# Kernel optimization log

Measured on AMD Instinct MI355X. Metric: run time of the kernel, lower is better.

## Reference

```python
import jax, jax.numpy as jnp
import numpy as np

N = 100000      # nodes
IN = 64         # in_channels
HID = 64        # hidden_channels
H2 = HID // 2   # per-sign channels
E = 1600000     # edges per sign


def _mean_aggr(x_src, edge_index, num_nodes):
    """Mean of x_src[src] scattered onto dst (PyG mean aggregation)."""
    src, dst = edge_index[0], edge_index[1]
    s = jax.ops.segment_sum(x_src[src], dst, num_segments=num_nodes)
    cnt = jax.ops.segment_sum(jnp.ones((src.shape[0],), x_src.dtype), dst,
                              num_segments=num_nodes)
    return s / jnp.maximum(cnt, 1.0)[:, None]


def setup_inputs() -> dict:
    key = jax.random.key(0)
    ks = jax.random.split(key, 12)
    x = jax.random.normal(ks[0], (N, IN), jnp.float32)
    pos_edge_index = jax.random.randint(ks[1], (2, E), 0, N)
    neg_edge_index = jax.random.randint(ks[2], (2, E), 0, N)

    def w(k, fan_in, fan_out):
        b = 1.0 / np.sqrt(fan_in)
        return jax.random.uniform(k, (fan_in, fan_out), jnp.float32, -b, b)

    return dict(
        x=x, pos_edge_index=pos_edge_index, neg_edge_index=neg_edge_index,
        # conv1 (first_aggr=True): lin_l (no bias applied via l), lin_r (bias)
        w1_pl=w(ks[3], IN, H2), w1_pr=w(ks[4], IN, H2), b1_p=jnp.zeros((H2,), jnp.float32),
        w1_nl=w(ks[5], IN, H2), w1_nr=w(ks[6], IN, H2), b1_n=jnp.zeros((H2,), jnp.float32),
        # conv2 (first_aggr=False): lin_l over cat of two aggregations (2*H2), lin_r over H2
        w2_pl=w(ks[7], 2 * H2, H2), w2_pr=w(ks[8], H2, H2), b2_p=jnp.zeros((H2,), jnp.float32),
        w2_nl=w(ks[9], 2 * H2, H2), w2_nr=w(ks[10], H2, H2), b2_n=jnp.zeros((H2,), jnp.float32),
    )


def reference(x, pos_edge_index, neg_edge_index,
              w1_pl, w1_pr, b1_p, w1_nl, w1_nr, b1_n,
              w2_pl, w2_pr, b2_p, w2_nl, w2_nr, b2_n):
    n = x.shape[0]
    # --- conv1, first_aggr=True ---
    agg_p = _mean_aggr(x, pos_edge_index, n)          # [N, IN]
    agg_n = _mean_aggr(x, neg_edge_index, n)
    out_pos = agg_p @ w1_pl + x @ w1_pr + b1_p         # [N, H2]
    out_neg = agg_n @ w1_nl + x @ w1_nr + b1_n
    z = jax.nn.relu(jnp.concatenate([out_pos, out_neg], axis=-1))  # [N, HID]

    # --- conv2, first_aggr=False ---
    h2 = z.shape[-1] // 2
    zp, zn = z[:, :h2], z[:, h2:]
    p1 = _mean_aggr(zp, pos_edge_index, n)
    p2 = _mean_aggr(zn, neg_edge_index, n)
    out_pos = jnp.concatenate([p1, p2], axis=-1) @ w2_pl + zp @ w2_pr + b2_p
    n1 = _mean_aggr(zn, pos_edge_index, n)
    n2 = _mean_aggr(zp, neg_edge_index, n)
    out_neg = jnp.concatenate([n1, n2], axis=-1) @ w2_nl + zn @ w2_nr + b2_n
    z = jax.nn.relu(jnp.concatenate([out_pos, out_neg], axis=-1))  # [N, HID]
    return z
```

## Files before the change

kernel.cpp:

```cpp
#include <hip/hip_runtime.h>
#include <hip/hip_fp16.h>

using uint = unsigned int;

static constexpr int NN  = 100000;
static constexpr int NE  = 1600000;
static constexpr int DIM = 64;
static constexpr int HH  = 32;
static constexpr int NBLK = (NN + 255) / 256;
static constexpr int HB   = 256;
static constexpr int CHUNK = NE / HB;
static constexpr int BSH  = 8;
static constexpr int BSZ  = 256;
static constexpr int NBKT = (NN + BSZ - 1) / BSZ;

__device__ __forceinline__ float2 up16(uint v) {
  __half2 h = *reinterpret_cast<__half2*>(&v);
  return __half22float2(h);
}
__device__ __forceinline__ uint pk16(float a, float b) {
  __half2 h = __floats2half2_rn(a, b);
  return *reinterpret_cast<uint*>(&h);
}


__global__ void c_hist(const int* __restrict__ pe, const int* __restrict__ ne,
                       int* __restrict__ part_hist) {
  const int set = blockIdx.y;
  const int* dstA = (set ? ne : pe) + NE;
  __shared__ int h[512];
  h[threadIdx.x] = 0; h[threadIdx.x + 256] = 0;
  __syncthreads();
  int lo = blockIdx.x * CHUNK;
  int hi = lo + CHUNK;
  for (int i = lo + threadIdx.x; i < hi; i += 256)
    atomicAdd(&h[dstA[i] >> BSH], 1);
  __syncthreads();
  int* o = part_hist + (size_t)(set * HB + blockIdx.x) * 512;
  o[threadIdx.x] = h[threadIdx.x];
  o[threadIdx.x + 256] = h[threadIdx.x + 256];
}

__global__ void c_colscan(int* __restrict__ part_hist, int* __restrict__ tot) {
  const int set = blockIdx.y;
  const int k   = blockIdx.x;
  const int t   = threadIdx.x;
  int v = part_hist[(size_t)(set * HB + t) * 512 + k];
  __shared__ int sm[256];
  sm[t] = v;
  __syncthreads();
  for (int off = 1; off < 256; off <<= 1) {
    int add = (t >= off) ? sm[t - off] : 0;
    __syncthreads();
    sm[t] += add;
    __syncthreads();
  }
  part_hist[(size_t)(set * HB + t) * 512 + k] = (t == 0) ? 0 : sm[t - 1];
  if (t == 255) tot[set * 512 + k] = sm[255];
}

__global__ void c_basescan(const int* __restrict__ tot, int* __restrict__ base) {
  const int t   = threadIdx.x;
  const int seg = t >> 9;
  const int idx = t & 511;
  int v = tot[seg * 512 + idx];
  __shared__ int sm[1024];
  sm[t] = v;
  __syncthreads();
  for (int off = 1; off < 512; off <<= 1) {
    int add = (idx >= off) ? sm[t - off] : 0;
    __syncthreads();
    sm[t] += add;
    __syncthreads();
  }
  base[seg * 513 + idx] = (idx == 0) ? 0 : sm[t - 1];
  if (idx == 511) base[seg * 513 + 512] = sm[t];
}

__global__ void c_scatpre(const int* __restrict__ pe, const int* __restrict__ ne,
                          const int* __restrict__ part_hist, const int* __restrict__ base,
                          uint* __restrict__ partP, uint* __restrict__ partN,
                          const float* __restrict__ x,
                          const float* __restrict__ w1_pl, const float* __restrict__ w1_pr,
                          const float* __restrict__ b1_p,
                          const float* __restrict__ w1_nl, const float* __restrict__ w1_nr,
                          const float* __restrict__ b1_n,
                          uint* __restrict__ y1p, uint* __restrict__ y1n,
                          float* __restrict__ r1) {
  __shared__ uint smem[4096];
  const int bx = blockIdx.x;
  const int t  = threadIdx.x;

  if (bx < 512) {
    const int set = bx >> 8;
    const int b   = bx & 255;
    const int* srcA = set ? ne : pe;
    const int* dstA = srcA + NE;
    uint* part = set ? partN : partP;
    int* off = (int*)smem;
    const int* ph = part_hist + (size_t)(set * HB + b) * 512;
    off[t]       = base[set * 513 + t]       + ph[t];
    off[t + 256] = base[set * 513 + t + 256] + ph[t + 256];
    __syncthreads();
    int lo = b * CHUNK;
    int hi = lo + CHUNK;
    for (int i = lo + t; i < hi; i += 256) {
      int src = srcA[i];
      int dst = dstA[i];
      int pos = atomicAdd(&off[dst >> BSH], 1);
      part[pos] = ((uint)src << BSH) | (uint)(dst & (BSZ - 1));
    }
    return;
  }

  const int pb   = bx - 512;
  const int h    = (pb >= NBLK) ? 1 : 0;
  const int nblk = pb - (h ? NBLK : 0);
  const float* wl   = h ? w1_nl : w1_pl;
  const float* wr   = h ? w1_nr : w1_pr;
  const float* bias = h ? b1_n  : b1_p;

  float* s_wl = (float*)smem;
  float* s_wr = (float*)smem + 2048;
  for (int i = t; i < DIM * HH; i += 256) {
    s_wl[i] = wl[i];
    s_wr[i] = wr[i];
  }
  __syncthreads();

  int node = nblk * 256 + t;
  if (node >= NN) return;

  float ay[HH], ar[HH];
#pragma unroll
  for (int j = 0; j < HH; ++j) { ay[j] = 0.f; ar[j] = bias[j]; }

  const float4* xrow = (const float4*)(x + (size_t)node * DIM);
#pragma unroll 4
  for (int k4 = 0; k4 < DIM / 4; ++k4) {
    float4 xv = xrow[k4];
#pragma unroll
    for (int u = 0; u < 4; ++u) {
      int k = k4 * 4 + u;
      float xk = (&xv.x)[u];
#pragma unroll
      for (int j = 0; j < HH; ++j) {
        ay[j] += xk * s_wl[k * HH + j];
        ar[j] += xk * s_wr[k * HH + j];
      }
    }
  }

  uint*  yo = (h ? y1n : y1p) + (size_t)node * 16;
  float* ro = r1 + (size_t)node * 64 + h * 32;
#pragma unroll
  for (int j = 0; j < 16; ++j) yo[j] = pk16(ay[2 * j], ay[2 * j + 1]);
#pragma unroll
  for (int j = 0; j < HH; ++j) ro[j] = ar[j];
}

__global__ void c_bucket(const uint* __restrict__ partP, const uint* __restrict__ partN,
                         const int* __restrict__ base,
                         int* __restrict__ row_p, int* __restrict__ row_n,
                         int* __restrict__ col_p, int* __restrict__ col_n) {
  const int bx = blockIdx.x;
  const int t  = threadIdx.x;
  const int set = (bx >= NBKT) ? 1 : 0;
  const int k   = bx - (set ? NBKT : 0);
  const uint* part = set ? partN : partP;
  int* row = set ? row_n : row_p;
  int* col = set ? col_n : col_p;
  const int lo = k * BSZ;
  const int hi = min(lo + BSZ, NN);
  const int s = base[set * 513 + k];
  const int e = base[set * 513 + k + 1];

  __shared__ int cnt[BSZ], rowl[BSZ], cnt2[BSZ];
  cnt[t] = 0; cnt2[t] = 0;
  __syncthreads();
  for (int i = s + t; i < e; i += 256)
    atomicAdd(&cnt[part[i] & (BSZ - 1)], 1);
  __syncthreads();
  rowl[t] = cnt[t];
  __syncthreads();
  for (int off = 1; off < BSZ; off <<= 1) {
    int a0 = (t >= off) ? rowl[t - off] : 0;
    __syncthreads();
    rowl[t] += a0;
    __syncthreads();
  }
  if (lo + t < hi) row[lo + t] = s + (t ? rowl[t - 1] : 0);
  if (k == NBKT - 1 && t == 0) row[NN] = NE;
  for (int i = s + t; i < e; i += 256) {
    uint p = part[i];
    int l = p & (BSZ - 1);
    int pos = s + (l ? rowl[l - 1] : 0) + atomicAdd(&cnt2[l], 1);
    col[pos] = (int)(p >> BSH);
  }
}

__global__ void k_aggr1(const uint* __restrict__ y1p, const uint* __restrict__ y1n,
                        const int* __restrict__ rp, const int* __restrict__ cp,
                        const int* __restrict__ rn, const int* __restrict__ cn,
                        const float* r1,
                        float* z) {
  int gid  = blockIdx.x * 256 + threadIdx.x;
  int node = gid >> 6;
  if (node >= NN) return;
  int lane = threadIdx.x & 63;
  int g = lane >> 2;
  int f = lane & 3;

  int s = rp[node], e = rp[node + 1];
  float a[8];
#pragma unroll
  for (int j = 0; j < 8; ++j) a[j] = 0.f;
  for (int i = s + g; i < e; i += 16) {
    int c = cp[i];
    uint4 v = *(const uint4*)&y1p[(size_t)c * 16 + 4 * f];
    float2 p0 = up16(v.x), p1 = up16(v.y), p2 = up16(v.z), p3 = up16(v.w);
    a[0] += p0.x; a[1] += p0.y; a[2] += p1.x; a[3] += p1.y;
    a[4] += p2.x; a[5] += p2.y; a[6] += p3.x; a[7] += p3.y;
  }
#pragma unroll
  for (int w = 4; w <= 32; w <<= 1) {
#pragma unroll
    for (int j = 0; j < 8; ++j) a[j] += __shfl_xor(a[j], w);
  }
  float invp = 1.f / (float)max(e - s, 1);

  s = rn[node]; e = rn[node + 1];
  float b[8];
#pragma unroll
  for (int j = 0; j < 8; ++j) b[j] = 0.f;
  for (int i = s + g; i < e; i += 16) {
    int c = cn[i];
    uint4 v = *(const uint4*)&y1n[(size_t)c * 16 + 4 * f];
    float2 p0 = up16(v.x), p1 = up16(v.y), p2 = up16(v.z), p3 = up16(v.w);
    b[0] += p0.x; b[1] += p0.y; b[2] += p1.x; b[3] += p1.y;
    b[4] += p2.x; b[5] += p2.y; b[6] += p3.x; b[7] += p3.y;
  }
#pragma unroll
  for (int w = 4; w <= 32; w <<= 1) {
#pragma unroll
    for (int j = 0; j < 8; ++j) b[j] += __shfl_xor(b[j], w);
  }
  float invn = 1.f / (float)max(e - s, 1);

  size_t base = (size_t)node * 64;
  if (g == 0) {
    const float4 r0 = *(const float4*)(r1 + base + 8 * f);
    const float4 r1v = *(const float4*)(r1 + base + 8 * f + 4);
    float4 o0, o1;
    o0.x = fmaxf(a[0] * invp + r0.x, 0.f);
    o0.y = fmaxf(a[1] * invp + r0.y, 0.f);
    o0.z = fmaxf(a[2] * invp + r0.z, 0.f);
    o0.w = fmaxf(a[3] * invp + r0.w, 0.f);
    o1.x = fmaxf(a[4] * invp + r1v.x, 0.f);
    o1.y = fmaxf(a[5] * invp + r1v.y, 0.f);
    o1.z = fmaxf(a[6] * invp + r1v.z, 0.f);
    o1.w = fmaxf(a[7] * invp + r1v.w, 0.f);
    *(float4*)(z + base + 8 * f) = o0;
    *(float4*)(z + base + 8 * f + 4) = o1;
  } else if (g == 1) {
    const float4 r0 = *(const float4*)(r1 + base + 32 + 8 * f);
    const float4 r1v = *(const float4*)(r1 + base + 32 + 8 * f + 4);
    float4 o0, o1;
    o0.x = fmaxf(b[0] * invn + r0.x, 0.f);
    o0.y = fmaxf(b[1] * invn + r0.y, 0.f);
    o0.z = fmaxf(b[2] * invn + r0.z, 0.f);
    o0.w = fmaxf(b[3] * invn + r0.w, 0.f);
    o1.x = fmaxf(b[4] * invn + r1v.x, 0.f);
    o1.y = fmaxf(b[5] * invn + r1v.y, 0.f);
    o1.z = fmaxf(b[6] * invn + r1v.z, 0.f);
    o1.w = fmaxf(b[7] * invn + r1v.w, 0.f);
    *(float4*)(z + base + 32 + 8 * f) = o0;
    *(float4*)(z + base + 32 + 8 * f + 4) = o1;
  }
}

__global__ void k_mid(const float* __restrict__ z,
                      const float* __restrict__ w2_pl, const float* __restrict__ w2_pr,
                      const float* __restrict__ b2_p,
                      const float* __restrict__ w2_nl, const float* __restrict__ w2_nr,
                      const float* __restrict__ b2_n,
                      uint* __restrict__ u_pos, uint* __restrict__ u_neg,
                      float* __restrict__ r2) {
  const int t = blockIdx.y;
  const float* mat;
  const float* bias = nullptr;
  int srcHalf;
  switch (t) {
    case 0: mat = w2_pl;            srcHalf = 0; break;
    case 1: mat = w2_nl;            srcHalf = 1; break;
    case 2: mat = w2_pl + 32 * 32;  srcHalf = 1; break;
    case 3: mat = w2_nl + 32 * 32;  srcHalf = 0; break;
    case 4: mat = w2_pr; bias = b2_p; srcHalf = 0; break;
    default: mat = w2_nr; bias = b2_n; srcHalf = 1; break;
  }

  __shared__ float s_m[HH][HH];
  for (int i = threadIdx.x; i < HH * HH; i += 256) s_m[i >> 5][i & 31] = mat[i];
  __syncthreads();

  int node = blockIdx.x * 256 + threadIdx.x;
  if (node >= NN) return;

  float acc[HH];
#pragma unroll
  for (int j = 0; j < HH; ++j) acc[j] = bias ? bias[j] : 0.f;

  const float4* zrow = (const float4*)(z + (size_t)node * 64 + srcHalf * 32);
#pragma unroll 4
  for (int k4 = 0; k4 < HH / 4; ++k4) {
    float4 v = zrow[k4];
#pragma unroll
    for (int u = 0; u < 4; ++u) {
      int k = k4 * 4 + u;
      float vv = (&v.x)[u];
#pragma unroll
      for (int j = 0; j < HH; ++j) acc[j] += vv * s_m[k][j];
    }
  }

  if (t < 4) {
    uint* o = (t < 2 ? u_pos : u_neg) + (size_t)node * 32 + (t & 1) * 16;
#pragma unroll
    for (int j = 0; j < 16; ++j) o[j] = pk16(acc[2 * j], acc[2 * j + 1]);
  } else {
    float* o = r2 + (size_t)node * 64 + (t - 4) * 32;
#pragma unroll
    for (int j = 0; j < HH; ++j) o[j] = acc[j];
  }
}

__global__ void k_aggr2(const uint* __restrict__ u_pos, const uint* __restrict__ u_neg,
                        const int* __restrict__ rp, const int* __restrict__ cp,
                        const int* __restrict__ rn, const int* __restrict__ cn,
                        const float* __restrict__ r2,
                        float* __restrict__ out) {
  int gid  = blockIdx.x * 256 + threadIdx.x;
  int node = gid >> 6;
  if (node >= NN) return;
  int lane = threadIdx.x & 63;
  int g = lane >> 3;
  int f = lane & 7;

  int s = rp[node], e = rp[node + 1];
  float a[8];
#pragma unroll
  for (int j = 0; j < 8; ++j) a[j] = 0.f;
  for (int i = s + g; i < e; i += 8) {
    int c = cp[i];
    uint4 v = *(const uint4*)&u_pos[(size_t)c * 32 + 4 * f];
    float2 p0 = up16(v.x), p1 = up16(v.y), p2 = up16(v.z), p3 = up16(v.w);
    a[0] += p0.x; a[1] += p0.y; a[2] += p1.x; a[3] += p1.y;
    a[4] += p2.x; a[5] += p2.y; a[6] += p3.x; a[7] += p3.y;
  }
#pragma unroll
  for (int w = 8; w <= 32; w <<= 1) {
#pragma unroll
    for (int j = 0; j < 8; ++j) a[j] += __shfl_xor(a[j], w);
  }
  float invp = 1.f / (float)max(e - s, 1);

  s = rn[node]; e = rn[node + 1];
  float b[8];
#pragma unroll
  for (int j = 0; j < 8; ++j) b[j] = 0.f;
  for (int i = s + g; i < e; i += 8) {
    int c = cn[i];
    uint4 v = *(const uint4*)&u_neg[(size_t)c * 32 + 4 * f];
    float2 p0 = up16(v.x), p1 = up16(v.y), p2 = up16(v.z), p3 = up16(v.w);
    b[0] += p0.x; b[1] += p0.y; b[2] += p1.x; b[3] += p1.y;
    b[4] += p2.x; b[5] += p2.y; b[6] += p3.x; b[7] += p3.y;
  }
#pragma unroll
  for (int w = 8; w <= 32; w <<= 1) {
#pragma unroll
    for (int j = 0; j < 8; ++j) b[j] += __shfl_xor(b[j], w);
  }
  float invn = 1.f / (float)max(e - s, 1);

  if (g == 0) {
    size_t base = (size_t)node * 64 + 8 * f;
    const float4 r0 = *(const float4*)(r2 + base);
    const float4 r1v = *(const float4*)(r2 + base + 4);
    float4 o0, o1;
    o0.x = fmaxf(a[0] * invp + b[0] * invn + r0.x, 0.f);
    o0.y = fmaxf(a[1] * invp + b[1] * invn + r0.y, 0.f);
    o0.z = fmaxf(a[2] * invp + b[2] * invn + r0.z, 0.f);
    o0.w = fmaxf(a[3] * invp + b[3] * invn + r0.w, 0.f);
    o1.x = fmaxf(a[4] * invp + b[4] * invn + r1v.x, 0.f);
    o1.y = fmaxf(a[5] * invp + b[5] * invn + r1v.y, 0.f);
    o1.z = fmaxf(a[6] * invp + b[6] * invn + r1v.z, 0.f);
    o1.w = fmaxf(a[7] * invp + b[7] * invn + r1v.w, 0.f);
    *(float4*)(out + base) = o0;
    *(float4*)(out + base + 4) = o1;
  }
}


extern "C" void kernel_launch(void* const* d_in, const int* in_sizes, int n_in,
                              void* d_out, int out_size, void* d_ws, size_t ws_size,
                              hipStream_t stream) {
  const float* x     = (const float*)d_in[0];
  const int*   pe    = (const int*)d_in[1];
  const int*   ne    = (const int*)d_in[2];
  const float* w1_pl = (const float*)d_in[3];
  const float* w1_pr = (const float*)d_in[4];
  const float* b1_p  = (const float*)d_in[5];
  const float* w1_nl = (const float*)d_in[6];
  const float* w1_nr = (const float*)d_in[7];
  const float* b1_n  = (const float*)d_in[8];
  const float* w2_pl = (const float*)d_in[9];
  const float* w2_pr = (const float*)d_in[10];
  const float* b2_p  = (const float*)d_in[11];
  const float* w2_nl = (const float*)d_in[12];
  const float* w2_nr = (const float*)d_in[13];
  const float* b2_n  = (const float*)d_in[14];

  char* ws = (char*)d_ws;
  size_t off = 0;
  auto alloc = [&](size_t bytes) -> char* {
    char* p = ws + off;
    off = (off + bytes + 255) & ~(size_t)255;
    return p;
  };

  int* row_p = (int*)alloc((size_t)(NN + 1) * 4);
  int* row_n = (int*)alloc((size_t)(NN + 1) * 4);
  int* col_p = (int*)alloc((size_t)NE * 4);
  int* col_n = (int*)alloc((size_t)NE * 4);
  int* part_hist = (int*)alloc((size_t)2 * HB * 512 * 4);
  int* tot   = (int*)alloc((size_t)2 * 512 * 4);
  int* base  = (int*)alloc((size_t)2 * 513 * 4);

  char* regA  = alloc((size_t)NN * 64 * 4);
  uint* partP = (uint*)regA;
  uint* partN = (uint*)(regA + (size_t)NE * 4);
  uint* u_pos = (uint*)regA;
  uint* u_neg = (uint*)(regA + (size_t)NN * 32 * 4);

  char*  regB = alloc((size_t)NN * 64 * 4);
  uint*  y1p  = (uint*)regB;
  uint*  y1n  = (uint*)(regB + (size_t)NN * 16 * 4);
  float* r2   = (float*)regB;

  float* r1 = (float*)d_out;
  float* z  = (float*)d_out;

  const int nb = NBLK;
  const int ab = (NN * 64 + 255) / 256;

  dim3 hg(HB, 2);
  c_hist<<<hg, 256, 0, stream>>>(pe, ne, part_hist);
  dim3 cg(512, 2);
  c_colscan<<<cg, 256, 0, stream>>>(part_hist, tot);
  c_basescan<<<1, 1024, 0, stream>>>(tot, base);
  c_scatpre<<<512 + 2 * NBLK, 256, 0, stream>>>(
      pe, ne, part_hist, base, partP, partN,
      x, w1_pl, w1_pr, b1_p, w1_nl, w1_nr, b1_n, y1p, y1n, r1);
  c_bucket<<<2 * NBKT, 256, 0, stream>>>(partP, partN, base,
                                         row_p, row_n, col_p, col_n);

  k_aggr1<<<ab, 256, 0, stream>>>(y1p, y1n, row_p, col_p, row_n, col_n, r1, z);

  dim3 g2(nb, 6);
  k_mid<<<g2, 256, 0, stream>>>(z, w2_pl, w2_pr, b2_p, w2_nl, w2_nr, b2_n,
                                u_pos, u_neg, r2);

  k_aggr2<<<ab, 256, 0, stream>>>(u_pos, u_neg, row_p, col_p, row_n, col_n, r2,
                                  (float*)d_out);
}
```

Measured before the change: 304.0 us.

## Use more histogram/scatter blocks and split layer-1 precompute into its own kernel

Raises the number of edge-partition blocks from 256 to 1024 per sign, so the histogram and scatter passes spread across more CUs with smaller chunks, and widens the column scan to 1024 threads. The layer-1 dense transform is pulled out of the combined scatter kernel into a separate kernel launched first, so the scatter no longer shares a grid with divergent matmul blocks. part_hist moves into the regA workspace region after the partition buffers. The larger histogram costs more scan work and memory, and there is one extra launch.

After: 330.3 us. 1.09x slower.

```diff
diff --git a/kernel.cpp b/kernel.cpp
--- a/kernel.cpp
+++ b/kernel.cpp
@@ -8,8 +8,8 @@
 static constexpr int DIM = 64;
 static constexpr int HH  = 32;
 static constexpr int NBLK = (NN + 255) / 256;
-static constexpr int HB   = 256;
-static constexpr int CHUNK = NE / HB;
+static constexpr int HB   = 1024;
+static constexpr int CHUNK = (NE + HB - 1) / HB;
 static constexpr int BSH  = 8;
 static constexpr int BSZ  = 256;
 static constexpr int NBKT = (NN + BSZ - 1) / BSZ;
@@ -32,7 +32,7 @@
   h[threadIdx.x] = 0; h[threadIdx.x + 256] = 0;
   __syncthreads();
   int lo = blockIdx.x * CHUNK;
-  int hi = lo + CHUNK;
+  int hi = min(lo + CHUNK, NE);
   for (int i = lo + threadIdx.x; i < hi; i += 256)
     atomicAdd(&h[dstA[i] >> BSH], 1);
   __syncthreads();
@@ -46,17 +46,17 @@
   const int k   = blockIdx.x;
   const int t   = threadIdx.x;
   int v = part_hist[(size_t)(set * HB + t) * 512 + k];
-  __shared__ int sm[256];
+  __shared__ int sm[HB];
   sm[t] = v;
   __syncthreads();
-  for (int off = 1; off < 256; off <<= 1) {
+  for (int off = 1; off < HB; off <<= 1) {
     int add = (t >= off) ? sm[t - off] : 0;
     __syncthreads();
     sm[t] += add;
     __syncthreads();
   }
   part_hist[(size_t)(set * HB + t) * 512 + k] = (t == 0) ? 0 : sm[t - 1];
-  if (t == 255) tot[set * 512 + k] = sm[255];
+  if (t == HB - 1) tot[set * 512 + k] = sm[HB - 1];
 }
 
 __global__ void c_basescan(const int* __restrict__ tot, int* __restrict__ base) {
@@ -77,86 +77,27 @@
   if (idx == 511) base[seg * 513 + 512] = sm[t];
 }
 
-__global__ void c_scatpre(const int* __restrict__ pe, const int* __restrict__ ne,
+__global__ void c_scatter(const int* __restrict__ pe, const int* __restrict__ ne,
                           const int* __restrict__ part_hist, const int* __restrict__ base,
-                          uint* __restrict__ partP, uint* __restrict__ partN,
-                          const float* __restrict__ x,
-                          const float* __restrict__ w1_pl, const float* __restrict__ w1_pr,
-                          const float* __restrict__ b1_p,
-                          const float* __restrict__ w1_nl, const float* __restrict__ w1_nr,
-                          const float* __restrict__ b1_n,
-                          uint* __restrict__ y1p, uint* __restrict__ y1n,
-                          float* __restrict__ r1) {
-  __shared__ uint smem[4096];
-  const int bx = blockIdx.x;
-  const int t  = threadIdx.x;
-
-  if (bx < 512) {
-    const int set = bx >> 8;
-    const int b   = bx & 255;
-    const int* srcA = set ? ne : pe;
-    const int* dstA = srcA + NE;
-    uint* part = set ? partN : partP;
-    int* off = (int*)smem;
-    const int* ph = part_hist + (size_t)(set * HB + b) * 512;
-    off[t]       = base[set * 513 + t]       + ph[t];
-    off[t + 256] = base[set * 513 + t + 256] + ph[t + 256];
-    __syncthreads();
-    int lo = b * CHUNK;
-    int hi = lo + CHUNK;
-    for (int i = lo + t; i < hi; i += 256) {
-      int src = srcA[i];
-      int dst = dstA[i];
-      int pos = atomicAdd(&off[dst >> BSH], 1);
-      part[pos] = ((uint)src << BSH) | (uint)(dst & (BSZ - 1));
-    }
-    return;
-  }
-
-  const int pb   = bx - 512;
-  const int h    = (pb >= NBLK) ? 1 : 0;
-  const int nblk = pb - (h ? NBLK : 0);
-  const float* wl   = h ? w1_nl : w1_pl;
-  const float* wr   = h ? w1_nr : w1_pr;
-  const float* bias = h ? b1_n  : b1_p;
-
-  float* s_wl = (float*)smem;
-  float* s_wr = (float*)smem + 2048;
-  for (int i = t; i < DIM * HH; i += 256) {
-    s_wl[i] = wl[i];
-    s_wr[i] = wr[i];
-  }
-  __syncthreads();
-
-  int node = nblk * 256 + t;
-  if (node >= NN) return;
-
-  float ay[HH], ar[HH];
-#pragma unroll
-  for (int j = 0; j < HH; ++j) { ay[j] = 0.f; ar[j] = bias[j]; }
-
-  const float4* xrow = (const float4*)(x + (size_t)node * DIM);
-#pragma unroll 4
-  for (int k4 = 0; k4 < DIM / 4; ++k4) {
-    float4 xv = xrow[k4];
-#pragma unroll
-    for (int u = 0; u < 4; ++u) {
-      int k = k4 * 4 + u;
-      float xk = (&xv.x)[u];
-#pragma unroll
-      for (int j = 0; j < HH; ++j) {
-        ay[j] += xk * s_wl[k * HH + j];
-        ar[j] += xk * s_wr[k * HH + j];
-      }
-    }
-  }
-
-  uint*  yo = (h ? y1n : y1p) + (size_t)node * 16;
-  float* ro = r1 + (size_t)node * 64 + h * 32;
-#pragma unroll
-  for (int j = 0; j < 16; ++j) yo[j] = pk16(ay[2 * j], ay[2 * j + 1]);
-#pragma unroll
-  for (int j = 0; j < HH; ++j) ro[j] = ar[j];
+                          uint* __restrict__ partP, uint* __restrict__ partN) {
+  const int set = blockIdx.y;
+  const int b   = blockIdx.x;
+  const int* srcA = set ? ne : pe;
+  const int* dstA = srcA + NE;
+  uint* part = set ? partN : partP;
+  __shared__ int off[512];
+  const int* ph = part_hist + (size_t)(set * HB + b) * 512;
+  off[threadIdx.x]       = base[set * 513 + threadIdx.x]       + ph[threadIdx.x];
+  off[threadIdx.x + 256] = base[set * 513 + threadIdx.x + 256] + ph[threadIdx.x + 256];
+  __syncthreads();
+  int lo = b * CHUNK;
+  int hi = min(lo + CHUNK, NE);
+  for (int i = lo + threadIdx.x; i < hi; i += 256) {
+    int src = srcA[i];
+    int dst = dstA[i];
+    int pos = atomicAdd(&off[dst >> BSH], 1);
+    part[pos] = ((uint)src << BSH) | (uint)(dst & (BSZ - 1));
+  }
 }
 
 __global__ void c_bucket(const uint* __restrict__ partP, const uint* __restrict__ partN,
@@ -197,6 +138,57 @@
     int pos = s + (l ? rowl[l - 1] : 0) + atomicAdd(&cnt2[l], 1);
     col[pos] = (int)(p >> BSH);
   }
+}
+
+__global__ void k_pre1(const float* __restrict__ x,
+                       const float* __restrict__ w1_pl, const float* __restrict__ w1_pr,
+                       const float* __restrict__ b1_p,
+                       const float* __restrict__ w1_nl, const float* __restrict__ w1_nr,
+                       const float* __restrict__ b1_n,
+                       uint* __restrict__ y1p, uint* __restrict__ y1n,
+                       float* __restrict__ r1) {
+  const int h = blockIdx.y;
+  const float* wl   = h ? w1_nl : w1_pl;
+  const float* wr   = h ? w1_nr : w1_pr;
+  const float* bias = h ? b1_n  : b1_p;
+
+  __shared__ float s_wl[DIM * HH];
+  __shared__ float s_wr[DIM * HH];
+  for (int i = threadIdx.x; i < DIM * HH; i += 256) {
+    s_wl[i] = wl[i];
+    s_wr[i] = wr[i];
+  }
+  __syncthreads();
+
+  int node = blockIdx.x * 256 + threadIdx.x;
+  if (node >= NN) return;
+
+  float ay[HH], ar[HH];
+#pragma unroll
+  for (int j = 0; j < HH; ++j) { ay[j] = 0.f; ar[j] = bias[j]; }
+
+  const float4* xrow = (const float4*)(x + (size_t)node * DIM);
+#pragma unroll 4
+  for (int k4 = 0; k4 < DIM / 4; ++k4) {
+    float4 xv = xrow[k4];
+#pragma unroll
+    for (int u = 0; u < 4; ++u) {
+      int k = k4 * 4 + u;
+      float xk = (&xv.x)[u];
+#pragma unroll
+      for (int j = 0; j < HH; ++j) {
+        ay[j] += xk * s_wl[k * HH + j];
+        ar[j] += xk * s_wr[k * HH + j];
+      }
+    }
+  }
+
+  uint*  yo = (h ? y1n : y1p) + (size_t)node * 16;
+  float* ro = r1 + (size_t)node * 64 + h * 32;
+#pragma unroll
+  for (int j = 0; j < 16; ++j) yo[j] = pk16(ay[2 * j], ay[2 * j + 1]);
+#pragma unroll
+  for (int j = 0; j < HH; ++j) ro[j] = ar[j];
 }
 
 __global__ void k_aggr1(const uint* __restrict__ y1p, const uint* __restrict__ y1n,
@@ -432,13 +424,13 @@
   int* row_n = (int*)alloc((size_t)(NN + 1) * 4);
   int* col_p = (int*)alloc((size_t)NE * 4);
   int* col_n = (int*)alloc((size_t)NE * 4);
-  int* part_hist = (int*)alloc((size_t)2 * HB * 512 * 4);
   int* tot   = (int*)alloc((size_t)2 * 512 * 4);
   int* base  = (int*)alloc((size_t)2 * 513 * 4);
 
   char* regA  = alloc((size_t)NN * 64 * 4);
   uint* partP = (uint*)regA;
   uint* partN = (uint*)(regA + (size_t)NE * 4);
+  int*  part_hist = (int*)(regA + (size_t)2 * NE * 4);
   uint* u_pos = (uint*)regA;
   uint* u_neg = (uint*)(regA + (size_t)NN * 32 * 4);
 
@@ -453,14 +445,16 @@
   const int nb = NBLK;
   const int ab = (NN * 64 + 255) / 256;
 
+  dim3 pg(nb, 2);
+  k_pre1<<<pg, 256, 0, stream>>>(x, w1_pl, w1_pr, b1_p, w1_nl, w1_nr, b1_n,
+                                 y1p, y1n, r1);
+
   dim3 hg(HB, 2);
   c_hist<<<hg, 256, 0, stream>>>(pe, ne, part_hist);
   dim3 cg(512, 2);
-  c_colscan<<<cg, 256, 0, stream>>>(part_hist, tot);
+  c_colscan<<<cg, HB, 0, stream>>>(part_hist, tot);
   c_basescan<<<1, 1024, 0, stream>>>(tot, base);
-  c_scatpre<<<512 + 2 * NBLK, 256, 0, stream>>>(
-      pe, ne, part_hist, base, partP, partN,
-      x, w1_pl, w1_pr, b1_p, w1_nl, w1_nr, b1_n, y1p, y1n, r1);
+  c_scatter<<<hg, 256, 0, stream>>>(pe, ne, part_hist, base, partP, partN);
   c_bucket<<<2 * NBKT, 256, 0, stream>>>(partP, partN, base,
                                          row_p, row_n, col_p, col_n);
 
```
